# Optimization experiments

Hardware: AMD Instinct MI355X
Metric: run time of the kernel (lower is better)

The kernel has to match this reference:

```python
import jax, jax.numpy as jnp
import numpy as np

NA = 100000   # author nodes
NP = 100000   # paper nodes
E = 500000    # edges per relation
H = 128       # hidden size
FA = 256      # author input features
FP = 128      # paper input features
LA = 4        # author labels
LP = 7        # paper labels


def setup_inputs() -> dict:
    key = jax.random.key(0)
    ks = iter(jax.random.split(key, 48))
    def rn(shape, scale=0.05):
        return jax.random.normal(next(ks), shape, jnp.float32) * scale
    inp = {}
    inp['x_author'] = jax.random.normal(next(ks), (NA, FA), jnp.float32)
    inp['x_paper'] = jax.random.normal(next(ks), (NP, FP), jnp.float32)
    inp['edge_index_p2a'] = jax.random.randint(next(ks), (2, E), 0, 100000, jnp.int64)  # row0: paper src, row1: author dst
    inp['edge_index_a2p'] = jax.random.randint(next(ks), (2, E), 0, 100000, jnp.int64)  # row0: author src, row1: paper dst
    # layer 1 convs (per message type): lin_src, lin_dst, lin_update(2H->H)
    inp['w1_p2a_src'] = rn((FP, H)); inp['b1_p2a_src'] = rn((H,))
    inp['w1_p2a_dst'] = rn((FA, H)); inp['b1_p2a_dst'] = rn((H,))
    inp['w1_p2a_upd'] = rn((2 * H, H)); inp['b1_p2a_upd'] = rn((H,))
    inp['w1_a2p_src'] = rn((FA, H)); inp['b1_a2p_src'] = rn((H,))
    inp['w1_a2p_dst'] = rn((FP, H)); inp['b1_a2p_dst'] = rn((H,))
    inp['w1_a2p_upd'] = rn((2 * H, H)); inp['b1_a2p_upd'] = rn((H,))
    # layer 2 convs (all dims = H)
    inp['w2_p2a_src'] = rn((H, H)); inp['b2_p2a_src'] = rn((H,))
    inp['w2_p2a_dst'] = rn((H, H)); inp['b2_p2a_dst'] = rn((H,))
    inp['w2_p2a_upd'] = rn((2 * H, H)); inp['b2_p2a_upd'] = rn((H,))
    inp['w2_a2p_src'] = rn((H, H)); inp['b2_a2p_src'] = rn((H,))
    inp['w2_a2p_dst'] = rn((H, H)); inp['b2_a2p_dst'] = rn((H,))
    inp['w2_a2p_upd'] = rn((2 * H, H)); inp['b2_a2p_upd'] = rn((H,))
    # batchnorm affine params per node type per layer
    inp['g1_a'] = jnp.ones((H,), jnp.float32); inp['be1_a'] = jnp.zeros((H,), jnp.float32)
    inp['g1_p'] = jnp.ones((H,), jnp.float32); inp['be1_p'] = jnp.zeros((H,), jnp.float32)
    inp['g2_a'] = jnp.ones((H,), jnp.float32); inp['be2_a'] = jnp.zeros((H,), jnp.float32)
    inp['g2_p'] = jnp.ones((H,), jnp.float32); inp['be2_p'] = jnp.zeros((H,), jnp.float32)
    # post message-passing heads
    inp['w_post_a'] = rn((H, LA)); inp['b_post_a'] = rn((LA,))
    inp['w_post_p'] = rn((H, LP)); inp['b_post_p'] = rn((LP,))
    return inp


def _mean_agg(x_src, src, dst, n_dst):
    # gather source features along edges, mean-scatter to destination nodes
    msg = x_src[src]                                            # [E, F]
    s = jax.ops.segment_sum(msg, dst, num_segments=n_dst)       # [n_dst, F]
    cnt = jax.ops.segment_sum(jnp.ones((dst.shape[0],), msg.dtype), dst, num_segments=n_dst)
    return s / jnp.maximum(cnt, 1.0)[:, None]


def _conv(x_src, x_dst, src, dst, ws, bs, wd, bd, wu, bu):
    agg = _mean_agg(x_src, src, dst, x_dst.shape[0])
    h = jnp.concatenate([x_dst @ wd + bd, agg @ ws + bs], axis=-1)   # [n_dst, 2H]
    return h @ wu + bu


def _bn_lrelu(x, g, b):
    # BatchNorm1d(eps=1) in training mode (batch stats, biased var) then LeakyReLU(0.01)
    m = x.mean(axis=0)
    v = x.var(axis=0)
    y = g * (x - m) / jnp.sqrt(v + 1.0) + b
    return jnp.where(y >= 0, y, 0.01 * y)


def reference(x_author, x_paper, edge_index_p2a, edge_index_a2p,
              w1_p2a_src, b1_p2a_src, w1_p2a_dst, b1_p2a_dst, w1_p2a_upd, b1_p2a_upd,
              w1_a2p_src, b1_a2p_src, w1_a2p_dst, b1_a2p_dst, w1_a2p_upd, b1_a2p_upd,
              w2_p2a_src, b2_p2a_src, w2_p2a_dst, b2_p2a_dst, w2_p2a_upd, b2_p2a_upd,
              w2_a2p_src, b2_a2p_src, w2_a2p_dst, b2_a2p_dst, w2_a2p_upd, b2_a2p_upd,
              g1_a, be1_a, g1_p, be1_p, g2_a, be2_a, g2_p, be2_p,
              w_post_a, b_post_a, w_post_p, b_post_p):
    src_pa, dst_pa = edge_index_p2a[0], edge_index_p2a[1]
    src_ap, dst_ap = edge_index_a2p[0], edge_index_a2p[1]
    # layer 1: per-message-type conv -> per-node-type BN + LeakyReLU
    h_a = _conv(x_paper, x_author, src_pa, dst_pa, w1_p2a_src, b1_p2a_src, w1_p2a_dst, b1_p2a_dst, w1_p2a_upd, b1_p2a_upd)
    h_p = _conv(x_author, x_paper, src_ap, dst_ap, w1_a2p_src, b1_a2p_src, w1_a2p_dst, b1_a2p_dst, w1_a2p_upd, b1_a2p_upd)
    h_a = _bn_lrelu(h_a, g1_a, be1_a)
    h_p = _bn_lrelu(h_p, g1_p, be1_p)
    # layer 2
    h_a2 = _conv(h_p, h_a, src_pa, dst_pa, w2_p2a_src, b2_p2a_src, w2_p2a_dst, b2_p2a_dst, w2_p2a_upd, b2_p2a_upd)
    h_p2 = _conv(h_a, h_p, src_ap, dst_ap, w2_a2p_src, b2_a2p_src, w2_a2p_dst, b2_a2p_dst, w2_a2p_upd, b2_a2p_upd)
    h_a2 = _bn_lrelu(h_a2, g2_a, be2_a)
    h_p2 = _bn_lrelu(h_p2, g2_p, be2_p)
    # post message-passing heads per node type
    out_a = h_a2 @ w_post_a + b_post_a   # [NA, LA]
    out_p = h_p2 @ w_post_p + b_post_p   # [NP, LP]
    return (out_a, out_p)
```

## Files before the change

kernel.cpp:

```cpp
#include <hip/hip_runtime.h>

#define NN 100000
#define NE 500000
#define HD 128
#define NBLK 391

typedef float f32x4v __attribute__((ext_vector_type(4)));
typedef short s16x8  __attribute__((ext_vector_type(8)));

#define QS 2048.0f
#define IQS (1.0f/2048.0f)

static __device__ __forceinline__ short enc1(float v){
  float x = v * QS;
  x = fminf(32767.f, fmaxf(-32767.f, x));
  return (short)__float2int_rn(x);
}
static __device__ __forceinline__ short4 enc4(float4 v){
  short4 s; s.x = enc1(v.x); s.y = enc1(v.y); s.z = enc1(v.z); s.w = enc1(v.w);
  return s;
}
static __device__ __forceinline__ float4 dec4(short4 q){
  return make_float4(q.x*IQS, q.y*IQS, q.z*IQS, q.w*IQS);
}
static __device__ __forceinline__ void dec8v(s16x8 q, f32x4v& v0, f32x4v& v1){
  #pragma unroll
  for (int j = 0; j < 4; ++j) v0[j] = (float)q[j] * IQS;
  #pragma unroll
  for (int j = 0; j < 4; ++j) v1[j] = (float)q[4+j] * IQS;
}

static __device__ __forceinline__ unsigned f2bf_bits(float f){
  unsigned u = __float_as_uint(f);
  return (u + 0x7FFF + ((u >> 16) & 1)) >> 16;
}
static __device__ __forceinline__ void split8v(f32x4v v0, f32x4v v1, s16x8& hi, s16x8& lo){
  #pragma unroll
  for (int j = 0; j < 4; ++j){
    float f = v0[j];
    unsigned hb = f2bf_bits(f);
    hi[j] = (short)hb; lo[j] = (short)f2bf_bits(f - __uint_as_float(hb << 16));
  }
  #pragma unroll
  for (int j = 0; j < 4; ++j){
    float f = v1[j];
    unsigned hb = f2bf_bits(f);
    hi[4+j] = (short)hb; lo[4+j] = (short)f2bf_bits(f - __uint_as_float(hb << 16));
  }
}

static __device__ __forceinline__ float4 bn_lrelu4(float4 v, float4 sc, float4 sh){
  v.x = v.x*sc.x + sh.x; v.x = v.x >= 0.f ? v.x : 0.01f*v.x;
  v.y = v.y*sc.y + sh.y; v.y = v.y >= 0.f ? v.y : 0.01f*v.y;
  v.z = v.z*sc.z + sh.z; v.z = v.z >= 0.f ? v.z : 0.01f*v.z;
  v.w = v.w*sc.w + sh.w; v.w = v.w >= 0.f ? v.w : 0.01f*v.w;
  return v;
}
static __device__ __forceinline__ f32x4v bn_lrelu4v(f32x4v v, f32x4v sc, f32x4v sh){
  #pragma unroll
  for (int j = 0; j < 4; ++j){
    float y = v[j]*sc[j] + sh[j];
    v[j] = y >= 0.f ? y : 0.01f*y;
  }
  return v;
}

__global__ void k_count(const int* __restrict__ ei_pa, const int* __restrict__ ei_ap,
                        int* __restrict__ deg2){
  int idx = blockIdx.x * 256 + threadIdx.x;
  if (idx < NE)        atomicAdd(&deg2[      ei_pa[NE + idx]], 1);
  else if (idx < 2*NE) atomicAdd(&deg2[NN + ei_ap[NE + (idx - NE)]], 1);
}

__global__ void k_bsum(const int* __restrict__ deg2, int* __restrict__ bsum){
  int rel = blockIdx.x / NBLK, b = blockIdx.x % NBLK;
  int i = b*256 + threadIdx.x;
  int v = (i < NN) ? deg2[rel*NN + i] : 0;
  __shared__ int s[256];
  s[threadIdx.x] = v; __syncthreads();
  for (int o = 128; o > 0; o >>= 1){
    if (threadIdx.x < o) s[threadIdx.x] += s[threadIdx.x + o];
    __syncthreads();
  }
  if (threadIdx.x == 0) bsum[rel*512 + b] = s[0];
}

__global__ void k_bscan(const int* __restrict__ bsum, int* __restrict__ bsoff){
  int rel = blockIdx.x, t = threadIdx.x;
  int v = (t < NBLK) ? bsum[rel*512 + t] : 0;
  __shared__ int s[512];
  s[t] = v; __syncthreads();
  for (int o = 1; o < 512; o <<= 1){
    int x = (t >= o) ? s[t - o] : 0;
    __syncthreads();
    s[t] += x;
    __syncthreads();
  }
  bsoff[rel*512 + t] = s[t] - v;
}

__global__ void k_scanC(const int* __restrict__ deg2, const int* __restrict__ bsoff,
                        int* __restrict__ off2, int* __restrict__ cur2){
  int rel = blockIdx.x / NBLK, b = blockIdx.x % NBLK;
  int i = b*256 + threadIdx.x, t = threadIdx.x;
  int v = (i < NN) ? deg2[rel*NN + i] : 0;
  __shared__ int s[256];
  s[t] = v; __syncthreads();
  for (int o = 1; o < 256; o <<= 1){
    int x = (t >= o) ? s[t - o] : 0;
    __syncthreads();
    s[t] += x;
    __syncthreads();
  }
  if (i < NN){
    int o = bsoff[rel*512 + b] + s[t] - v;
    off2[rel*NN + i] = o;
    cur2[rel*NN + i] = o;
  }
}

__global__ void k_fill(const int* __restrict__ ei_pa, const int* __restrict__ ei_ap,
                       int* __restrict__ cur2,
                       int* __restrict__ col_pa, int* __restrict__ col_ap){
  int idx = blockIdx.x * 256 + threadIdx.x;
  if (idx < NE){
    int s = ei_pa[idx], d = ei_pa[NE + idx];
    int pos = atomicAdd(&cur2[d], 1);
    col_pa[pos] = s;
  } else if (idx < 2*NE){
    int e = idx - NE;
    int s = ei_ap[e], d = ei_ap[NE + e];
    int pos = atomicAdd(&cur2[NN + d], 1);
    col_ap[pos] = s;
  }
}

struct FoldDesc { const float* A; const float* B; short* T; int off; };
struct FoldArgs { FoldDesc d[8]; int rs[9]; };

__global__ void k_fold(FoldArgs fa){
  int row = blockIdx.x;
  int seg = 0;
  #pragma unroll
  for (int s = 0; s < 8; ++s) if (row >= fa.rs[s+1]) seg = s + 1;
  int m = row - fa.rs[seg];
  const float* A = fa.d[seg].A + (size_t)m * 128;
  const float* B = fa.d[seg].B;
  int n = threadIdx.x;
  float acc = 0.f;
  for (int k = 0; k < 128; ++k) acc += A[k] * B[k*128 + n];
  unsigned hb = f2bf_bits(acc);
  float hf = __uint_as_float(hb << 16);
  unsigned lb = f2bf_bits(acc - hf);
  int gkc = fa.d[seg].off + (m >> 5), quad = (m >> 3) & 3, j = m & 7;
  int lane = quad*16 + (n & 15), nt = n >> 4;
  size_t fb = (size_t)((gkc*8 + nt)*2)*512 + lane*8 + j;
  fa.d[seg].T[fb]       = (short)hb;
  fa.d[seg].T[fb + 512] = (short)lb;
}

struct BiasArgs { const float* bd[4]; const float* bs[4]; const float* wu[4];
                  const float* bu[4]; float* outb[4]; };
__global__ void k_biasfold(BiasArgs ba){
  int s = blockIdx.x, j = threadIdx.x;
  const float* wu = ba.wu[s];
  float acc = ba.bu[s][j];
  for (int k = 0; k < 128; ++k)
    acc += ba.bd[s][k] * wu[k*128 + j] + ba.bs[s][k] * wu[(128 + k)*128 + j];
  ba.outb[s][j] = acc;
}

template<int A1Q, int DUALB, int BN>
__global__ __launch_bounds__(256)
void k_gemm4(const void* __restrict__ A1v, int lda1, int KC1,
             const float* __restrict__ bn1,
             const short* __restrict__ A2, int lda2, int KC2,
             const short* __restrict__ BfA, const short* __restrict__ BfB,
             const float* __restrict__ bias, const short* __restrict__ extra,
             short* __restrict__ C, short* __restrict__ C2,
             float* __restrict__ stats, int M)
{
  constexpr int LDSSZ = 32768 + (BN ? 1024 : 0);
  __shared__ __align__(16) char smem[LDSSZ];
  float* bnlds = (float*)(smem + 32768);

  const int tid  = threadIdx.x;
  const int wave = tid >> 6, lane = tid & 63;
  const int li   = lane & 15, quad = lane >> 4;
  const int rowT = blockIdx.x * 128 + wave * 32;
  const int KCtot = KC1 + KC2;

  f32x4v acc1[2][8];
  f32x4v acc2[2][8];
  #pragma unroll
  for (int mt = 0; mt < 2; ++mt)
    #pragma unroll
    for (int nt = 0; nt < 8; ++nt){
      acc1[mt][nt] = (f32x4v){0.f, 0.f, 0.f, 0.f};
      if (DUALB) acc2[mt][nt] = (f32x4v){0.f, 0.f, 0.f, 0.f};
    }

  const void*  b1[2];
  const short* b2[2];
  #pragma unroll
  for (int mt = 0; mt < 2; ++mt){
    int row = rowT + mt*16 + li;
    int r = (row < M) ? row : 0;
    if (A1Q) b1[mt] = (const void*)((const short*)A1v + (size_t)r*lda1 + quad*8);
    else     b1[mt] = (const void*)((const float*)A1v + (size_t)r*lda1 + quad*8);
    b2[mt] = A2 ? (A2 + (size_t)r*lda2 + quad*8) : (const short*)nullptr;
  }

  auto loadA = [&](int gkc, f32x4v (&dst)[2][2]){
    #pragma unroll
    for (int mt = 0; mt < 2; ++mt){
      if (gkc < KC1){
        if (A1Q){
          const short* p = (const short*)b1[mt] + gkc*32;
          dst[mt][0] = *(const f32x4v*)p;
        } else {
          const float* p = (const float*)b1[mt] + gkc*32;
          dst[mt][0] = *(const f32x4v*)p;
          dst[mt][1] = *(const f32x4v*)(p + 4);
        }
      } else {
        const short* p = b2[mt] + (gkc - KC1)*32;
        dst[mt][0] = *(const f32x4v*)p;
      }
    }
  };

  auto stage = [&](int g){
    if (!DUALB){
      const char* s = (const char*)BfA + (size_t)g * 16384;
      #pragma unroll
      for (int c = 0; c < 8; ++c){
        int off = c*4096 + wave*1024;
        __builtin_amdgcn_global_load_lds(
            (const __attribute__((address_space(1))) unsigned int*)(s + off + lane*16),
            (__attribute__((address_space(3))) unsigned int*)(smem + off),
            16, 0, 0);
      }
    } else {
      const char* sA = (const char*)BfA + (size_t)g * 16384;
      #pragma unroll
      for (int c = 0; c < 4; ++c){
        int off = c*4096 + wave*1024;
        __builtin_amdgcn_global_load_lds(
            (const __attribute__((address_space(1))) unsigned int*)(sA + off + lane*16),
            (__attribute__((address_space(3))) unsigned int*)(smem + off),
            16, 0, 0);
      }
      if (g < KC1){
        const char* sB = (const char*)BfB + (size_t)g * 16384;
        #pragma unroll
        for (int c = 0; c < 4; ++c){
          int off = c*4096 + wave*1024;
          __builtin_amdgcn_global_load_lds(
              (const __attribute__((address_space(1))) unsigned int*)(sB + off + lane*16),
              (__attribute__((address_space(3))) unsigned int*)(smem + 16384 + off),
              16, 0, 0);
        }
      }
    }
  };

  auto computeK = [&](int gkc, const short* base, f32x4v (&raw)[2][2]){
    s16x8 ah[2], al[2];
    #pragma unroll
    for (int mt = 0; mt < 2; ++mt){
      f32x4v v0, v1;
      if (A1Q || gkc >= KC1){
        dec8v(__builtin_bit_cast(s16x8, raw[mt][0]), v0, v1);
      } else {
        v0 = raw[mt][0]; v1 = raw[mt][1];
      }
      if (BN && gkc < KC1){
        int bb = gkc*32 + quad*8;
        f32x4v sc0 = *(const f32x4v*)(bnlds + bb);
        f32x4v sc1 = *(const f32x4v*)(bnlds + bb + 4);
        f32x4v sh0 = *(const f32x4v*)(bnlds + bb + 128);
        f32x4v sh1 = *(const f32x4v*)(bnlds + bb + 132);
        v0 = bn_lrelu4v(v0, sc0, sh0);
        v1 = bn_lrelu4v(v1, sc1, sh1);
      }
      split8v(v0, v1, ah[mt], al[mt]);
    }
    __builtin_amdgcn_s_setprio(1);
    #pragma unroll
    for (int nt = 0; nt < 8; ++nt){
      const short* bp = base + (nt << 10);
      s16x8 bh = *(const s16x8*)bp;
      s16x8 bl = *(const s16x8*)(bp + 512);
      #pragma unroll
      for (int mt = 0; mt < 2; ++mt){
        acc1[mt][nt] = __builtin_amdgcn_mfma_f32_16x16x32_bf16(ah[mt], bh, acc1[mt][nt], 0, 0, 0);
        acc1[mt][nt] = __builtin_amdgcn_mfma_f32_16x16x32_bf16(al[mt], bh, acc1[mt][nt], 0, 0, 0);
        acc1[mt][nt] = __builtin_amdgcn_mfma_f32_16x16x32_bf16(ah[mt], bl, acc1[mt][nt], 0, 0, 0);
      }
    }
    if (DUALB && gkc < KC1){
      const short* base2 = base + 8192;
      #pragma unroll
      for (int nt = 0; nt < 8; ++nt){
        const short* bp = base2 + (nt << 10);
        s16x8 bh = *(const s16x8*)bp;
        s16x8 bl = *(const s16x8*)(bp + 512);
        #pragma unroll
        for (int mt = 0; mt < 2; ++mt){
          acc2[mt][nt] = __builtin_amdgcn_mfma_f32_16x16x32_bf16(ah[mt], bh, acc2[mt][nt], 0, 0, 0);
          acc2[mt][nt] = __builtin_amdgcn_mfma_f32_16x16x32_bf16(al[mt], bh, acc2[mt][nt], 0, 0, 0);
          acc2[mt][nt] = __builtin_amdgcn_mfma_f32_16x16x32_bf16(ah[mt], bl, acc2[mt][nt], 0, 0, 0);
        }
      }
    }
    __builtin_amdgcn_s_setprio(0);
  };

  if (BN && tid < 256) bnlds[tid] = bn1[tid];
  f32x4v cur[2][2], nxt[2][2];
  loadA(0, cur);

  const int KCG = DUALB ? 1 : 2;
  for (int g = 0; g < KCtot; g += KCG){
    if (g) __syncthreads();
    stage(g);
    __syncthreads();
    #pragma unroll
    for (int kk = 0; kk < (DUALB ? 1 : 2); ++kk){
      int gkc = g + kk;
      if (gkc + 1 < KCtot) loadA(gkc + 1, nxt);
      const short* base = (const short*)smem + (DUALB ? 0 : kk*8192) + lane*8;
      computeK(gkc, base, cur);
      #pragma unroll
      for (int mt = 0; mt < 2; ++mt){
        cur[mt][0] = nxt[mt][0]; cur[mt][1] = nxt[mt][1];
      }
    }
  }

  __syncthreads();
  float* Cw = (float*)smem + wave*2048;
  int col4 = lane & 31;
  float4 s1 = make_float4(0.f,0.f,0.f,0.f), s2 = s1;

  auto epi_pass = [&](f32x4v (&ac)[2][8], short* Cout, const float* bptr,
                      bool wStats){
    float4 bias4 = make_float4(0.f,0.f,0.f,0.f);
    if (bptr) bias4 = ((const float4*)bptr)[col4];
    #pragma unroll
    for (int mt = 0; mt < 2; ++mt){
      #pragma unroll
      for (int r = 0; r < 4; ++r){
        int lr = quad*4 + r;
        #pragma unroll
        for (int nt = 0; nt < 8; ++nt){
          int c = nt*16 + li;
          int chunk = ((c >> 2) + 2*quad) & 31;
          Cw[lr*128 + chunk*4 + (c & 3)] = ac[mt][nt][r];
        }
      }
      #pragma unroll
      for (int i = 0; i < 8; ++i){
        int lr = i*2 + (lane >> 5);
        int grow = rowT + mt*16 + lr;
        if (grow >= M) continue;
        int chunk = (col4 + 2*(lr >> 2)) & 31;
        float4 v = *(const float4*)(Cw + lr*128 + chunk*4);
        v.x += bias4.x; v.y += bias4.y; v.z += bias4.z; v.w += bias4.w;
        if (extra && wStats){
          short4 q = *(const short4*)(extra + ((size_t)grow << 7) + col4*4);
          float4 e = dec4(q);
          v.x += e.x; v.y += e.y; v.z += e.z; v.w += e.w;
        }
        *(short4*)(Cout + ((size_t)grow << 7) + col4*4) = enc4(v);
        if (wStats){
          s1.x += v.x; s1.y += v.y; s1.z += v.z; s1.w += v.w;
          s2.x += v.x*v.x; s2.y += v.y*v.y; s2.z += v.z*v.z; s2.w += v.w*v.w;
        }
      }
    }
  };

  epi_pass(acc1, C, bias, true);
  if (DUALB) epi_pass(acc2, C2, nullptr, false);

  if (stats){
    __syncthreads();
    float* Ss = (float*)smem;
    ((float4*)Ss)[tid*2]     = s1;
    ((float4*)Ss)[tid*2 + 1] = s2;
    __syncthreads();
    int c = tid & 127, kind = tid >> 7;
    int cc4 = c >> 2, comp = c & 3;
    float s = 0.f;
    #pragma unroll
    for (int wv = 0; wv < 4; ++wv)
      #pragma unroll
      for (int hf = 0; hf < 2; ++hf)
        s += Ss[(wv*64 + hf*32 + cc4)*8 + kind*4 + comp];
    atomicAdd(&stats[kind*128 + c], s);
  }
}

template<int IS>
__global__ __launch_bounds__(256)
void k_agg(const void* __restrict__ tv, const int* __restrict__ off,
           const int* __restrict__ deg, const int* __restrict__ col,
           short* __restrict__ o, const float* __restrict__ bn){
  const float* tf = (const float*)tv;
  const short* ts = (const short*)tv;
  int slot = threadIdx.x >> 5, col4 = threadIdx.x & 31;
  int d = blockIdx.x*8 + slot;
  if (d >= NN) return;
  float4 sc4, sh4;
  bool hasbn = IS && (bn != nullptr);
  if (hasbn){ sc4 = ((const float4*)bn)[col4]; sh4 = ((const float4*)(bn+128))[col4]; }
  auto loadrow = [&](int row) -> float4 {
    float4 v;
    if (IS) v = dec4(*(const short4*)(ts + ((size_t)row << 7) + col4*4));
    else    v = ((const float4*)(tf + ((size_t)row << 7)))[col4];
    if (hasbn) v = bn_lrelu4(v, sc4, sh4);
    return v;
  };
  int s0 = off[d], cnt = deg[d];
  float4 a0 = make_float4(0.f,0.f,0.f,0.f), a1 = a0;
  int i = 0;
  for (; i + 4 <= cnt; i += 4){
    int sa = col[s0+i], sb = col[s0+i+1], sct = col[s0+i+2], sd = col[s0+i+3];
    float4 v0 = loadrow(sa);
    float4 v1 = loadrow(sb);
    float4 v2 = loadrow(sct);
    float4 v3 = loadrow(sd);
    a0.x += v0.x + v2.x; a0.y += v0.y + v2.y; a0.z += v0.z + v2.z; a0.w += v0.w + v2.w;
    a1.x += v1.x + v3.x; a1.y += v1.y + v3.y; a1.z += v1.z + v3.z; a1.w += v1.w + v3.w;
  }
  for (; i < cnt; ++i){
    float4 v0 = loadrow(col[s0+i]);
    a0.x += v0.x; a0.y += v0.y; a0.z += v0.z; a0.w += v0.w;
  }
  float inv = 1.0f / (float)(cnt > 0 ? cnt : 1);
  float4 r;
  r.x = (a0.x + a1.x)*inv; r.y = (a0.y + a1.y)*inv;
  r.z = (a0.z + a1.z)*inv; r.w = (a0.w + a1.w)*inv;
  *(short4*)(o + ((size_t)d << 7) + col4*4) = enc4(r);
}

__global__ void k_bnprep(const float* __restrict__ stats, const float* __restrict__ g,
                         const float* __restrict__ b, float* __restrict__ sc, int M){
  int c = threadIdx.x;
  float invN = 1.0f / (float)M;
  float m  = stats[c] * invN;
  float var = stats[128 + c] * invN - m*m;
  float scale = g[c] / sqrtf(var + 1.0f);
  sc[c] = scale;
  sc[128 + c] = b[c] - m*scale;
}

template<int LC>
__global__ void k_head(const short* __restrict__ h, const float* __restrict__ bn,
                       const float* __restrict__ w, const float* __restrict__ b,
                       float* __restrict__ o, int M){
  __shared__ float ws[128*LC];
  __shared__ float bs[LC];
  __shared__ float bsc[256];
  for (int i = threadIdx.x; i < 128*LC; i += 256) ws[i] = w[i];
  if (threadIdx.x < LC) bs[threadIdx.x] = b[threadIdx.x];
  if (threadIdx.x < 256) bsc[threadIdx.x] = bn[threadIdx.x];
  __syncthreads();
  int r = blockIdx.x*256 + threadIdx.x;
  if (r >= M) return;
  float acc[LC];
  #pragma unroll
  for (int c = 0; c < LC; ++c) acc[c] = bs[c];
  const short* hr = h + ((size_t)r << 7);
  for (int k4 = 0; k4 < 32; ++k4){
    float4 v = dec4(((const short4*)hr)[k4]);
    float4 sc = ((const float4*)bsc)[k4];
    float4 sh = ((const float4*)bsc)[32 + k4];
    v = bn_lrelu4(v, sc, sh);
    int k = k4*4;
    #pragma unroll
    for (int c = 0; c < LC; ++c)
      acc[c] += v.x*ws[k*LC+c] + v.y*ws[(k+1)*LC+c] + v.z*ws[(k+2)*LC+c] + v.w*ws[(k+3)*LC+c];
  }
  #pragma unroll
  for (int c = 0; c < LC; ++c) o[(size_t)r*LC + c] = acc[c];
}

extern "C" void kernel_launch(void* const* d_in, const int* in_sizes, int n_in,
                              void* d_out, int out_size, void* d_ws, size_t ws_size,
                              hipStream_t stream) {
  const float* x_author = (const float*)d_in[0];
  const float* x_paper  = (const float*)d_in[1];
  const int*   ei_pa    = (const int*)d_in[2];
  const int*   ei_ap    = (const int*)d_in[3];

  char* p = (char*)d_ws;
  auto alloc = [&](size_t bytes) -> void* {
    void* r = (void*)p; p += (bytes + 255) & ~(size_t)255; return r;
  };
  short* T_l1a  = (short*)alloc(12u*16384);
  short* T_l1ps = (short*)alloc( 8u*16384);
  short* T_l1pd = (short*)alloc( 4u*16384);
  short* T_l2a  = (short*)alloc( 8u*16384);
  short* T_l2p  = (short*)alloc( 8u*16384);
  float* w1a_b = (float*)alloc(128*4);      float* w1p_b = (float*)alloc(128*4);
  float* w2a_b = (float*)alloc(128*4);      float* w2p_b = (float*)alloc(128*4);
  float* stats4 = (float*)alloc(4*256*4);
  float* bnsc4  = (float*)alloc(4*256*4);
  int* deg2  = (int*)alloc(2*NN*4);
  int* off2  = (int*)alloc(2*NN*4);
  int* cur2  = (int*)alloc(2*NN*4);
  int* col_pa = (int*)alloc(NE*4);
  int* col_ap = (int*)alloc(NE*4);
  int* bsum  = (int*)alloc(1024*4);
  int* bsoff = (int*)alloc(1024*4);
  const size_t NB = (size_t)NN * 128;
  short* B1 = (short*)alloc(NB*2);
  short* B2 = (short*)alloc(NB*2);
  short* B3 = (short*)alloc(NB*2);
  short* B4 = (short*)alloc(NB*2);

  hipMemsetAsync(deg2, 0, 2*NN*4, stream);
  hipMemsetAsync(stats4, 0, 4*256*4, stream);
  k_count<<<(2*NE + 255)/256, 256, 0, stream>>>(ei_pa, ei_ap, deg2);
  k_bsum <<<2*NBLK, 256, 0, stream>>>(deg2, bsum);
  k_bscan<<<2, 512, 0, stream>>>(bsum, bsoff);
  k_scanC<<<2*NBLK, 256, 0, stream>>>(deg2, bsoff, off2, cur2);
  k_fill <<<(2*NE + 255)/256, 256, 0, stream>>>(ei_pa, ei_ap, cur2, col_pa, col_ap);

  FoldArgs fa;
  const float* wu1a = (const float*)d_in[8];
  const float* wu1p = (const float*)d_in[14];
  const float* wu2a = (const float*)d_in[20];
  const float* wu2p = (const float*)d_in[26];
  fa.d[0] = { (const float*)d_in[6],  wu1a,           T_l1a,  0 };
  fa.d[1] = { (const float*)d_in[4],  wu1a + 128*128, T_l1a,  8 };
  fa.d[2] = { (const float*)d_in[10], wu1p + 128*128, T_l1ps, 0 };
  fa.d[3] = { (const float*)d_in[12], wu1p,           T_l1pd, 0 };
  fa.d[4] = { (const float*)d_in[18], wu2a,           T_l2a,  0 };
  fa.d[5] = { (const float*)d_in[16], wu2a + 128*128, T_l2a,  4 };
  fa.d[6] = { (const float*)d_in[24], wu2p,           T_l2p,  0 };
  fa.d[7] = { (const float*)d_in[22], wu2p + 128*128, T_l2p,  4 };
  int rows[8] = {256,128,256,128,128,128,128,128};
  fa.rs[0] = 0;
  for (int i = 0; i < 8; ++i) fa.rs[i+1] = fa.rs[i] + rows[i];
  k_fold<<<fa.rs[8], 128, 0, stream>>>(fa);

  BiasArgs ba;
  ba.bd[0]=(const float*)d_in[7];  ba.bs[0]=(const float*)d_in[5];  ba.wu[0]=wu1a; ba.bu[0]=(const float*)d_in[9];  ba.outb[0]=w1a_b;
  ba.bd[1]=(const float*)d_in[13]; ba.bs[1]=(const float*)d_in[11]; ba.wu[1]=wu1p; ba.bu[1]=(const float*)d_in[15]; ba.outb[1]=w1p_b;
  ba.bd[2]=(const float*)d_in[19]; ba.bs[2]=(const float*)d_in[17]; ba.wu[2]=wu2a; ba.bu[2]=(const float*)d_in[21]; ba.outb[2]=w2a_b;
  ba.bd[3]=(const float*)d_in[25]; ba.bs[3]=(const float*)d_in[23]; ba.wu[3]=wu2p; ba.bu[3]=(const float*)d_in[27]; ba.outb[3]=w2p_b;
  k_biasfold<<<4, 128, 0, stream>>>(ba);

  const int GG = (NN + 127)/128;
  const int AGG_GRID = (NN + 7)/8;
  const int* off_pa = off2;        const int* deg_pa = deg2;
  const int* off_ap = off2 + NN;   const int* deg_ap = deg2 + NN;
  float* st_a1 = stats4;       float* st_p1 = stats4 + 256;
  float* st_a2 = stats4 + 512; float* st_p2 = stats4 + 768;
  float* sc_a1 = bnsc4;        float* sc_p1 = bnsc4 + 256;
  float* sc_a2 = bnsc4 + 512;  float* sc_p2 = bnsc4 + 768;

  k_agg<0><<<AGG_GRID, 256, 0, stream>>>(x_paper, off_pa, deg_pa, col_pa, B4, nullptr);
  k_gemm4<0,1,0><<<GG, 256, 0, stream>>>(
      x_author, 256, 8, nullptr, B4, 128, 4, T_l1a, T_l1ps, w1a_b,
      nullptr, B1, B3, st_a1, NN);
  k_bnprep<<<1, 128, 0, stream>>>(st_a1, (const float*)d_in[28], (const float*)d_in[29], sc_a1, NN);

  k_agg<1><<<AGG_GRID, 256, 0, stream>>>(B3, off_ap, deg_ap, col_ap, B4, nullptr);
  k_gemm4<0,0,0><<<GG, 256, 0, stream>>>(
      x_paper, 128, 4, nullptr, nullptr, 0, 0, T_l1pd, nullptr, w1p_b,
      B4, B2, nullptr, st_p1, NN);
  k_bnprep<<<1, 128, 0, stream>>>(st_p1, (const float*)d_in[30], (const float*)d_in[31], sc_p1, NN);

  k_agg<1><<<AGG_GRID, 256, 0, stream>>>(B2, off_pa, deg_pa, col_pa, B4, sc_p1);
  k_gemm4<1,0,1><<<GG, 256, 0, stream>>>(
      B1, 128, 4, sc_a1, B4, 128, 4, T_l2a, nullptr, w2a_b,
      nullptr, B3, nullptr, st_a2, NN);
  k_bnprep<<<1, 128, 0, stream>>>(st_a2, (const float*)d_in[32], (const float*)d_in[33], sc_a2, NN);
  k_head<4><<<(NN + 255)/256, 256, 0, stream>>>(B3, sc_a2, (const float*)d_in[36],
                                                (const float*)d_in[37], (float*)d_out, NN);

  k_agg<1><<<AGG_GRID, 256, 0, stream>>>(B1, off_ap, deg_ap, col_ap, B4, sc_a1);
  k_gemm4<1,0,1><<<GG, 256, 0, stream>>>(
      B2, 128, 4, sc_p1, B4, 128, 4, T_l2p, nullptr, w2p_b,
      nullptr, B1, nullptr, st_p2, NN);
  k_bnprep<<<1, 128, 0, stream>>>(st_p2, (const float*)d_in[34], (const float*)d_in[35], sc_p2, NN);
  k_head<7><<<(NN + 255)/256, 256, 0, stream>>>(B1, sc_p2, (const float*)d_in[38],
                                                (const float*)d_in[39], (float*)d_out + (size_t)NN*4, NN);
}
```

Before: 884.4 us.

## Pre-quantize input features to int16 and split dual-B GEMM into two single-B passes

Adds a k_quant kernel that converts x_author and x_paper to 16-bit fixed point once up front. Every GEMM and aggregation then reads shorts only, which halves input bandwidth and removes the float/short template variants. The fused dual-output layer-1 GEMM is replaced by two separate GEMM launches, so x_author is read twice but each launch uses fewer accumulators and the simpler double-chunk staging loop. The cost is extra quantization passes and buffers, and fixed-point rounding of the raw inputs with a scale of 2048 and clamping near ±16.

After: 835.7 us. 5.5% less time.

```diff
diff --git a/kernel.cpp b/kernel.cpp
--- a/kernel.cpp
+++ b/kernel.cpp
@@ -63,6 +63,15 @@
     v[j] = y >= 0.f ? y : 0.01f*y;
   }
   return v;
+}
+
+__global__ __launch_bounds__(256)
+void k_quant(const float* __restrict__ in, short* __restrict__ out, int n4){
+  int i = blockIdx.x*256 + threadIdx.x;
+  if (i < n4){
+    float4 v = ((const float4*)in)[i];
+    ((short4*)out)[i] = enc4(v);
+  }
 }
 
 __global__ void k_count(const int* __restrict__ ei_pa, const int* __restrict__ ei_ap,
@@ -170,15 +179,14 @@
   ba.outb[s][j] = acc;
 }
 
-template<int A1Q, int DUALB, int BN>
+template<int BN>
 __global__ __launch_bounds__(256)
-void k_gemm4(const void* __restrict__ A1v, int lda1, int KC1,
+void k_gemm5(const short* __restrict__ A1, int lda1, int KC1,
              const float* __restrict__ bn1,
              const short* __restrict__ A2, int lda2, int KC2,
-             const short* __restrict__ BfA, const short* __restrict__ BfB,
+             const short* __restrict__ Bf,
              const float* __restrict__ bias, const short* __restrict__ extra,
-             short* __restrict__ C, short* __restrict__ C2,
-             float* __restrict__ stats, int M)
+             short* __restrict__ C, float* __restrict__ stats, int M)
 {
   constexpr int LDSSZ = 32768 + (BN ? 1024 : 0);
   __shared__ __align__(16) char smem[LDSSZ];
@@ -190,91 +198,49 @@
   const int rowT = blockIdx.x * 128 + wave * 32;
   const int KCtot = KC1 + KC2;
 
-  f32x4v acc1[2][8];
-  f32x4v acc2[2][8];
+  f32x4v acc[2][8];
   #pragma unroll
   for (int mt = 0; mt < 2; ++mt)
     #pragma unroll
-    for (int nt = 0; nt < 8; ++nt){
-      acc1[mt][nt] = (f32x4v){0.f, 0.f, 0.f, 0.f};
-      if (DUALB) acc2[mt][nt] = (f32x4v){0.f, 0.f, 0.f, 0.f};
-    }
-
-  const void*  b1[2];
+    for (int nt = 0; nt < 8; ++nt)
+      acc[mt][nt] = (f32x4v){0.f, 0.f, 0.f, 0.f};
+
+  const short* b1[2];
   const short* b2[2];
   #pragma unroll
   for (int mt = 0; mt < 2; ++mt){
     int row = rowT + mt*16 + li;
     int r = (row < M) ? row : 0;
-    if (A1Q) b1[mt] = (const void*)((const short*)A1v + (size_t)r*lda1 + quad*8);
-    else     b1[mt] = (const void*)((const float*)A1v + (size_t)r*lda1 + quad*8);
+    b1[mt] = A1 + (size_t)r*lda1 + quad*8;
     b2[mt] = A2 ? (A2 + (size_t)r*lda2 + quad*8) : (const short*)nullptr;
   }
 
-  auto loadA = [&](int gkc, f32x4v (&dst)[2][2]){
+  auto loadA = [&](int gkc, f32x4v (&dst)[2]){
     #pragma unroll
     for (int mt = 0; mt < 2; ++mt){
-      if (gkc < KC1){
-        if (A1Q){
-          const short* p = (const short*)b1[mt] + gkc*32;
-          dst[mt][0] = *(const f32x4v*)p;
-        } else {
-          const float* p = (const float*)b1[mt] + gkc*32;
-          dst[mt][0] = *(const f32x4v*)p;
-          dst[mt][1] = *(const f32x4v*)(p + 4);
-        }
-      } else {
-        const short* p = b2[mt] + (gkc - KC1)*32;
-        dst[mt][0] = *(const f32x4v*)p;
-      }
+      const short* p = (gkc < KC1) ? (b1[mt] + gkc*32) : (b2[mt] + (gkc - KC1)*32);
+      dst[mt] = *(const f32x4v*)p;
     }
   };
 
   auto stage = [&](int g){
-    if (!DUALB){
-      const char* s = (const char*)BfA + (size_t)g * 16384;
-      #pragma unroll
-      for (int c = 0; c < 8; ++c){
-        int off = c*4096 + wave*1024;
-        __builtin_amdgcn_global_load_lds(
-            (const __attribute__((address_space(1))) unsigned int*)(s + off + lane*16),
-            (__attribute__((address_space(3))) unsigned int*)(smem + off),
-            16, 0, 0);
-      }
-    } else {
-      const char* sA = (const char*)BfA + (size_t)g * 16384;
-      #pragma unroll
-      for (int c = 0; c < 4; ++c){
-        int off = c*4096 + wave*1024;
-        __builtin_amdgcn_global_load_lds(
-            (const __attribute__((address_space(1))) unsigned int*)(sA + off + lane*16),
-            (__attribute__((address_space(3))) unsigned int*)(smem + off),
-            16, 0, 0);
-      }
-      if (g < KC1){
-        const char* sB = (const char*)BfB + (size_t)g * 16384;
-        #pragma unroll
-        for (int c = 0; c < 4; ++c){
-          int off = c*4096 + wave*1024;
-          __builtin_amdgcn_global_load_lds(
-              (const __attribute__((address_space(1))) unsigned int*)(sB + off + lane*16),
-              (__attribute__((address_space(3))) unsigned int*)(smem + 16384 + off),
-              16, 0, 0);
-        }
-      }
+    const char* s = (const char*)Bf + (size_t)g * 16384;
+    #pragma unroll
+    for (int c = 0; c < 8; ++c){
+      int off = c*4096 + wave*1024;
+      __builtin_amdgcn_global_load_lds(
+          (const __attribute__((address_space(1))) unsigned int*)(s + off + lane*16),
+          (__attribute__((address_space(3))) unsigned int*)(smem + off),
+          16, 0, 0);
     }
   };
 
-  auto computeK = [&](int gkc, const short* base, f32x4v (&raw)[2][2]){
+  auto computeK = [&](int gkc, const short* base, f32x4v (&raw)[2]){
     s16x8 ah[2], al[2];
     #pragma unroll
     for (int mt = 0; mt < 2; ++mt){
       f32x4v v0, v1;
-      if (A1Q || gkc >= KC1){
-        dec8v(__builtin_bit_cast(s16x8, raw[mt][0]), v0, v1);
-      } else {
-        v0 = raw[mt][0]; v1 = raw[mt][1];
-      }
+      dec8v(__builtin_bit_cast(s16x8, raw[mt]), v0, v1);
       if (BN && gkc < KC1){
         int bb = gkc*32 + quad*8;
         f32x4v sc0 = *(const f32x4v*)(bnlds + bb);
@@ -294,48 +260,28 @@
       s16x8 bl = *(const s16x8*)(bp + 512);
       #pragma unroll
       for (int mt = 0; mt < 2; ++mt){
-        acc1[mt][nt] = __builtin_amdgcn_mfma_f32_16x16x32_bf16(ah[mt], bh, acc1[mt][nt], 0, 0, 0);
-        acc1[mt][nt] = __builtin_amdgcn_mfma_f32_16x16x32_bf16(al[mt], bh, acc1[mt][nt], 0, 0, 0);
-        acc1[mt][nt] = __builtin_amdgcn_mfma_f32_16x16x32_bf16(ah[mt], bl, acc1[mt][nt], 0, 0, 0);
-      }
-    }
-    if (DUALB && gkc < KC1){
-      const short* base2 = base + 8192;
-      #pragma unroll
-      for (int nt = 0; nt < 8; ++nt){
-        const short* bp = base2 + (nt << 10);
-        s16x8 bh = *(const s16x8*)bp;
-        s16x8 bl = *(const s16x8*)(bp + 512);
-        #pragma unroll
-        for (int mt = 0; mt < 2; ++mt){
-          acc2[mt][nt] = __builtin_amdgcn_mfma_f32_16x16x32_bf16(ah[mt], bh, acc2[mt][nt], 0, 0, 0);
-          acc2[mt][nt] = __builtin_amdgcn_mfma_f32_16x16x32_bf16(al[mt], bh, acc2[mt][nt], 0, 0, 0);
-          acc2[mt][nt] = __builtin_amdgcn_mfma_f32_16x16x32_bf16(ah[mt], bl, acc2[mt][nt], 0, 0, 0);
-        }
+        acc[mt][nt] = __builtin_amdgcn_mfma_f32_16x16x32_bf16(ah[mt], bh, acc[mt][nt], 0, 0, 0);
+        acc[mt][nt] = __builtin_amdgcn_mfma_f32_16x16x32_bf16(al[mt], bh, acc[mt][nt], 0, 0, 0);
+        acc[mt][nt] = __builtin_amdgcn_mfma_f32_16x16x32_bf16(ah[mt], bl, acc[mt][nt], 0, 0, 0);
       }
     }
     __builtin_amdgcn_s_setprio(0);
   };
 
-  if (BN && tid < 256) bnlds[tid] = bn1[tid];
-  f32x4v cur[2][2], nxt[2][2];
+  if (BN) bnlds[tid] = bn1[tid];
+  f32x4v cur[2], nxt[2];
   loadA(0, cur);
 
-  const int KCG = DUALB ? 1 : 2;
-  for (int g = 0; g < KCtot; g += KCG){
+  for (int g = 0; g < KCtot; g += 2){
     if (g) __syncthreads();
     stage(g);
     __syncthreads();
     #pragma unroll
-    for (int kk = 0; kk < (DUALB ? 1 : 2); ++kk){
+    for (int kk = 0; kk < 2; ++kk){
       int gkc = g + kk;
       if (gkc + 1 < KCtot) loadA(gkc + 1, nxt);
-      const short* base = (const short*)smem + (DUALB ? 0 : kk*8192) + lane*8;
-      computeK(gkc, base, cur);
-      #pragma unroll
-      for (int mt = 0; mt < 2; ++mt){
-        cur[mt][0] = nxt[mt][0]; cur[mt][1] = nxt[mt][1];
-      }
+      computeK(gkc, (const short*)smem + kk*8192 + lane*8, cur);
+      cur[0] = nxt[0]; cur[1] = nxt[1];
     }
   }
 
@@ -343,48 +289,40 @@
   float* Cw = (float*)smem + wave*2048;
   int col4 = lane & 31;
   float4 s1 = make_float4(0.f,0.f,0.f,0.f), s2 = s1;
-
-  auto epi_pass = [&](f32x4v (&ac)[2][8], short* Cout, const float* bptr,
-                      bool wStats){
-    float4 bias4 = make_float4(0.f,0.f,0.f,0.f);
-    if (bptr) bias4 = ((const float4*)bptr)[col4];
-    #pragma unroll
-    for (int mt = 0; mt < 2; ++mt){
+  float4 bias4 = make_float4(0.f,0.f,0.f,0.f);
+  if (bias) bias4 = ((const float4*)bias)[col4];
+  #pragma unroll
+  for (int mt = 0; mt < 2; ++mt){
+    #pragma unroll
+    for (int r = 0; r < 4; ++r){
+      int lr = quad*4 + r;
       #pragma unroll
-      for (int r = 0; r < 4; ++r){
-        int lr = quad*4 + r;
-        #pragma unroll
-        for (int nt = 0; nt < 8; ++nt){
-          int c = nt*16 + li;
-          int chunk = ((c >> 2) + 2*quad) & 31;
-          Cw[lr*128 + chunk*4 + (c & 3)] = ac[mt][nt][r];
-        }
+      for (int nt = 0; nt < 8; ++nt){
+        int c = nt*16 + li;
+        int chunk = ((c >> 2) + 2*quad) & 31;
+        Cw[lr*128 + chunk*4 + (c & 3)] = acc[mt][nt][r];
       }
-      #pragma unroll
-      for (int i = 0; i < 8; ++i){
-        int lr = i*2 + (lane >> 5);
-        int grow = rowT + mt*16 + lr;
-        if (grow >= M) continue;
-        int chunk = (col4 + 2*(lr >> 2)) & 31;
-        float4 v = *(const float4*)(Cw + lr*128 + chunk*4);
-        v.x += bias4.x; v.y += bias4.y; v.z += bias4.z; v.w += bias4.w;
-        if (extra && wStats){
-          short4 q = *(const short4*)(extra + ((size_t)grow << 7) + col4*4);
-          float4 e = dec4(q);
-          v.x += e.x; v.y += e.y; v.z += e.z; v.w += e.w;
-        }
-        *(short4*)(Cout + ((size_t)grow << 7) + col4*4) = enc4(v);
-        if (wStats){
-          s1.x += v.x; s1.y += v.y; s1.z += v.z; s1.w += v.w;
-          s2.x += v.x*v.x; s2.y += v.y*v.y; s2.z += v.z*v.z; s2.w += v.w*v.w;
-        }
+    }
+    #pragma unroll
+    for (int i = 0; i < 8; ++i){
+      int lr = i*2 + (lane >> 5);
+      int grow = rowT + mt*16 + lr;
+      if (grow >= M) continue;
+      int chunk = (col4 + 2*(lr >> 2)) & 31;
+      float4 v = *(const float4*)(Cw + lr*128 + chunk*4);
+      v.x += bias4.x; v.y += bias4.y; v.z += bias4.z; v.w += bias4.w;
+      if (extra){
+        short4 q = *(const short4*)(extra + ((size_t)grow << 7) + col4*4);
+        float4 e = dec4(q);
+        v.x += e.x; v.y += e.y; v.z += e.z; v.w += e.w;
       }
-    }
-  };
-
-  epi_pass(acc1, C, bias, true);
-  if (DUALB) epi_pass(acc2, C2, nullptr, false);
-
+      *(short4*)(C + ((size_t)grow << 7) + col4*4) = enc4(v);
+      if (stats){
+        s1.x += v.x; s1.y += v.y; s1.z += v.z; s1.w += v.w;
+        s2.x += v.x*v.x; s2.y += v.y*v.y; s2.z += v.z*v.z; s2.w += v.w*v.w;
+      }
+    }
+  }
   if (stats){
     __syncthreads();
     float* Ss = (float*)smem;
@@ -403,23 +341,18 @@
   }
 }
 
-template<int IS>
 __global__ __launch_bounds__(256)
-void k_agg(const void* __restrict__ tv, const int* __restrict__ off,
+void k_agg(const short* __restrict__ t, const int* __restrict__ off,
            const int* __restrict__ deg, const int* __restrict__ col,
            short* __restrict__ o, const float* __restrict__ bn){
-  const float* tf = (const float*)tv;
-  const short* ts = (const short*)tv;
   int slot = threadIdx.x >> 5, col4 = threadIdx.x & 31;
   int d = blockIdx.x*8 + slot;
   if (d >= NN) return;
   float4 sc4, sh4;
-  bool hasbn = IS && (bn != nullptr);
+  bool hasbn = (bn != nullptr);
   if (hasbn){ sc4 = ((const float4*)bn)[col4]; sh4 = ((const float4*)(bn+128))[col4]; }
   auto loadrow = [&](int row) -> float4 {
-    float4 v;
-    if (IS) v = dec4(*(const short4*)(ts + ((size_t)row << 7) + col4*4));
-    else    v = ((const float4*)(tf + ((size_t)row << 7)))[col4];
+    float4 v = dec4(*(const short4*)(t + ((size_t)row << 7) + col4*4));
     if (hasbn) v = bn_lrelu4(v, sc4, sh4);
     return v;
   };
@@ -517,10 +450,15 @@
   int* bsum  = (int*)alloc(1024*4);
   int* bsoff = (int*)alloc(1024*4);
   const size_t NB = (size_t)NN * 128;
+  short* xa_q = (short*)alloc((size_t)NN*256*2);
+  short* xp_q = (short*)alloc(NB*2);
   short* B1 = (short*)alloc(NB*2);
   short* B2 = (short*)alloc(NB*2);
   short* B3 = (short*)alloc(NB*2);
   short* B4 = (short*)alloc(NB*2);
+
+  k_quant<<<(NN*64 + 255)/256, 256, 0, stream>>>(x_author, xa_q, NN*64);
+  k_quant<<<(NN*32 + 255)/256, 256, 0, stream>>>(x_paper,  xp_q, NN*32);
 
   hipMemsetAsync(deg2, 0, 2*NN*4, stream);
   hipMemsetAsync(stats4, 0, 4*256*4, stream);
@@ -564,30 +502,28 @@
   float* sc_a1 = bnsc4;        float* sc_p1 = bnsc4 + 256;
   float* sc_a2 = bnsc4 + 512;  float* sc_p2 = bnsc4 + 768;
 
-  k_agg<0><<<AGG_GRID, 256, 0, stream>>>(x_paper, off_pa, deg_pa, col_pa, B4, nullptr);
-  k_gemm4<0,1,0><<<GG, 256, 0, stream>>>(
-      x_author, 256, 8, nullptr, B4, 128, 4, T_l1a, T_l1ps, w1a_b,
-      nullptr, B1, B3, st_a1, NN);
+  k_agg<<<AGG_GRID, 256, 0, stream>>>(xp_q, off_pa, deg_pa, col_pa, B4, nullptr);
+  k_gemm5<0><<<GG, 256, 0, stream>>>(xa_q, 256, 8, nullptr, B4, 128, 4, T_l1a,
+                                     w1a_b, nullptr, B1, st_a1, NN);
   k_bnprep<<<1, 128, 0, stream>>>(st_a1, (const float*)d_in[28], (const float*)d_in[29], sc_a1, NN);
 
-  k_agg<1><<<AGG_GRID, 256, 0, stream>>>(B3, off_ap, deg_ap, col_ap, B4, nullptr);
-  k_gemm4<0,0,0><<<GG, 256, 0, stream>>>(
-      x_paper, 128, 4, nullptr, nullptr, 0, 0, T_l1pd, nullptr, w1p_b,
-      B4, B2, nullptr, st_p1, NN);
+  k_gemm5<0><<<GG, 256, 0, stream>>>(xa_q, 256, 8, nullptr, nullptr, 0, 0, T_l1ps,
+                                     nullptr, nullptr, B3, nullptr, NN);
+  k_agg<<<AGG_GRID, 256, 0, stream>>>(B3, off_ap, deg_ap, col_ap, B4, nullptr);
+  k_gemm5<0><<<GG, 256, 0, stream>>>(xp_q, 128, 4, nullptr, nullptr, 0, 0, T_l1pd,
+                                     w1p_b, B4, B2, st_p1, NN);
   k_bnprep<<<1, 128, 0, stream>>>(st_p1, (const float*)d_in[30], (const float*)d_in[31], sc_p1, NN);
 
-  k_agg<1><<<AGG_GRID, 256, 0, stream>>>(B2, off_pa, deg_pa, col_pa, B4, sc_p1);
-  k_gemm4<1,0,1><<<GG, 256, 0, stream>>>(
-      B1, 128, 4, sc_a1, B4, 128, 4, T_l2a, nullptr, w2a_b,
-      nullptr, B3, nullptr, st_a2, NN);
+  k_agg<<<AGG_GRID, 256, 0, stream>>>(B2, off_pa, deg_pa, col_pa, B4, sc_p1);
+  k_gemm5<1><<<GG, 256, 0, stream>>>(B1, 128, 4, sc_a1, B4, 128, 4, T_l2a,
+                                     w2a_b, nullptr, B3, st_a2, NN);
   k_bnprep<<<1, 128, 0, stream>>>(st_a2, (const float*)d_in[32], (const float*)d_in[33], sc_a2, NN);
   k_head<4><<<(NN + 255)/256, 256, 0, stream>>>(B3, sc_a2, (const float*)d_in[36],
                                                 (const float*)d_in[37], (float*)d_out, NN);
 
-  k_agg<1><<<AGG_GRID, 256, 0, stream>>>(B1, off_ap, deg_ap, col_ap, B4, sc_a1);
-  k_gemm4<1,0,1><<<GG, 256, 0, stream>>>(
-      B2, 128, 4, sc_p1, B4, 128, 4, T_l2p, nullptr, w2p_b,
-      nullptr, B1, nullptr, st_p2, NN);
+  k_agg<<<AGG_GRID, 256, 0, stream>>>(B1, off_ap, deg_ap, col_ap, B4, sc_a1);
+  k_gemm5<1><<<GG, 256, 0, stream>>>(B2, 128, 4, sc_p1, B4, 128, 4, T_l2p,
+                                     w2p_b, nullptr, B1, st_p2, NN);
   k_bnprep<<<1, 128, 0, stream>>>(st_p2, (const float*)d_in[34], (const float*)d_in[35], sc_p2, NN);
   k_head<7><<<(NN + 255)/256, 256, 0, stream>>>(B1, sc_p2, (const float*)d_in[38],
                                                 (const float*)d_in[39], (float*)d_out + (size_t)NN*4, NN);
```
